# Kernel tuning notes

Measured on AMD Instinct MI355X. Metric: run time of the kernel, lower is better.

## Reference

```python
import jax, jax.numpy as jnp
import numpy as np

V = 100000
NNZ = 1600000
B = 4
C_IN = 64
C_HID = 128
C_OUT = 64
K = 4
BN_EPS = 1e-5


def cheb_conv(x, rows, cols, vals, W, b):
    # x: (B, Cin, V); W: (K, Cin, Cout); b: (Cout,)
    Bn, Cin, Vn = x.shape
    Kn = W.shape[0]

    def spmm(y):  # y: (V, F) -> L @ y via edge-list scatter-add
        return jax.ops.segment_sum(vals[:, None] * y[cols], rows, num_segments=Vn)

    x0 = jnp.transpose(x, (2, 0, 1)).reshape(Vn, Bn * Cin)  # (V, B*Cin)
    xs = [x0]
    if Kn > 1:
        x1 = spmm(x0)
        xs.append(x1)
        for _ in range(2, Kn):
            x2 = 2.0 * spmm(x1) - x0  # Chebyshev recurrence
            xs.append(x2)
            x0, x1 = x1, x2
    Xk = jnp.stack(xs, 0).reshape(Kn, Vn, Bn, Cin)  # (K, V, B, Cin)
    out = jnp.einsum('kvbi,kio->bov', Xk, W)  # (B, Cout, V)
    return out + b[None, :, None]


def batch_norm(x, gamma, beta):
    # BatchNorm1d on (B, C, V): stats over (B, V), biased variance (training mode)
    mean = jnp.mean(x, axis=(0, 2), keepdims=True)
    var = jnp.mean(jnp.square(x - mean), axis=(0, 2), keepdims=True)
    xn = (x - mean) * jax.lax.rsqrt(var + BN_EPS)
    return xn * gamma[None, :, None] + beta[None, :, None]


def setup_inputs() -> dict:
    key = jax.random.key(0)
    ks = jax.random.split(key, 8)
    x = jax.random.normal(ks[0], (B, C_IN, V), dtype=jnp.float32)
    lap_rows = jax.random.randint(ks[1], (NNZ,), 0, V, dtype=jnp.int32)
    lap_cols = jax.random.randint(ks[2], (NNZ,), 0, V, dtype=jnp.int32)
    # scale so the effective Laplacian spectral norm is ~O(1) (Chebyshev assumes rescaled L)
    lap_vals = jax.random.normal(ks[3], (NNZ,), dtype=jnp.float32) * 0.01
    w1 = jax.random.normal(ks[4], (K, C_IN, C_HID), dtype=jnp.float32) * (1.0 / np.sqrt(K * C_IN))
    b1 = jnp.zeros((C_HID,), dtype=jnp.float32)
    bn_gamma = jnp.ones((C_HID,), dtype=jnp.float32)
    bn_beta = jnp.zeros((C_HID,), dtype=jnp.float32)
    w2 = jax.random.normal(ks[5], (K, C_HID, C_OUT), dtype=jnp.float32) * (1.0 / np.sqrt(K * C_HID))
    b2 = jnp.zeros((C_OUT,), dtype=jnp.float32)
    return {"x": x, "lap_rows": lap_rows, "lap_cols": lap_cols, "lap_vals": lap_vals,
            "w1": w1, "b1": b1, "bn_gamma": bn_gamma, "bn_beta": bn_beta,
            "w2": w2, "b2": b2}


def reference(x, lap_rows, lap_cols, lap_vals, w1, b1, bn_gamma, bn_beta, w2, b2):
    out = cheb_conv(x, lap_rows, lap_cols, lap_vals, w1, b1)
    out = jax.nn.relu(out)
    out = batch_norm(out, bn_gamma, bn_beta)
    out = cheb_conv(out, lap_rows, lap_cols, lap_vals, w2, b2)
    # in_channels == out_channels -> resizer is Identity
    return jax.nn.relu(out + x)
```

## Files before the change

### kernel.cpp

```cpp
#include <hip/hip_runtime.h>

#define V 100000
#define NNZ 1600000

typedef unsigned short ushort_t;
typedef unsigned int uint_t;
typedef __attribute__((ext_vector_type(4))) float f32x4;
typedef __attribute__((ext_vector_type(8))) short bf16x8;

__device__ __forceinline__ float bf2f(ushort_t u) {
    union { uint_t i; float f; } x; x.i = ((uint_t)u) << 16; return x.f;
}
__device__ __forceinline__ ushort_t f2bf(float f) {
    union { float f; uint_t i; } x; x.f = f;
    uint_t u = x.i;
    return (ushort_t)((u + 0x7fffu + ((u >> 16) & 1u)) >> 16);
}
__device__ __forceinline__ float blo(uint_t u) {
    union { uint_t i; float f; } x; x.i = u << 16; return x.f;
}
__device__ __forceinline__ float bhi(uint_t u) {
    union { uint_t i; float f; } x; x.i = u & 0xffff0000u; return x.f;
}
__device__ __forceinline__ uint_t pk(float a, float b) {
    return (uint_t)f2bf(a) | ((uint_t)f2bf(b) << 16);
}
__device__ __forceinline__ void unpack8(uint4 u, float* f) {
    f[0] = blo(u.x); f[1] = bhi(u.x); f[2] = blo(u.y); f[3] = bhi(u.y);
    f[4] = blo(u.z); f[5] = bhi(u.z); f[6] = blo(u.w); f[7] = bhi(u.w);
}
__device__ __forceinline__ uint4 pack8(const float* f) {
    uint4 u;
    u.x = pk(f[0], f[1]); u.y = pk(f[2], f[3]);
    u.z = pk(f[4], f[5]); u.w = pk(f[6], f[7]);
    return u;
}

__global__ void diag_k(float* __restrict__ out, float code) {
    if (threadIdx.x == 0 && blockIdx.x == 0) out[0] = code;
}

__global__ __launch_bounds__(256) void pack_x0_k(const float* __restrict__ x,
                                                 ushort_t* __restrict__ x0) {
    __shared__ float tile[32][33];
    int v0 = blockIdx.x * 32, j0 = blockIdx.y * 32;
    int tx = threadIdx.x & 31, ty = threadIdx.x >> 5;
    for (int jj = ty; jj < 32; jj += 8)
        tile[jj][tx] = x[(size_t)(j0 + jj) * V + v0 + tx];
    __syncthreads();
    for (int vv = ty; vv < 32; vv += 8)
        x0[(size_t)(v0 + vv) * 256 + j0 + tx] = f2bf(tile[tx][vv]);
}

__global__ __launch_bounds__(256) void prep_w_k(const float* __restrict__ w1,
                                                const float* __restrict__ w2,
                                                ushort_t* __restrict__ wp1,
                                                ushort_t* __restrict__ wp2) {
    int idx = blockIdx.x * 256 + threadIdx.x;
    if (idx < 32768) {
        int f = idx;
        int j = f & 7, ch = (f >> 3) & 127, q = (f >> 10) & 3, kb = (f >> 12) & 3, L = (f >> 14) & 1;
        int k = kb * 32 + q * 8 + j;
        int t = L * 2 + (k >> 6), i = k & 63;
        wp1[idx] = f2bf(w1[((size_t)t * 64 + i) * 128 + ch]);
    } else {
        int f = idx - 32768;
        int j = f & 7, o = (f >> 3) & 63, q = (f >> 9) & 3, kb = (f >> 11) & 3, t = (f >> 13) & 3;
        int k = kb * 32 + q * 8 + j;
        wp2[f] = f2bf(w2[((size_t)t * 128 + k) * 64 + o]);
    }
}

__global__ __launch_bounds__(256) void hist_k(const int* __restrict__ rows,
                                              int* __restrict__ counts) {
    int e = blockIdx.x * 256 + threadIdx.x;
    atomicAdd(&counts[rows[e]], 1);
}

__global__ __launch_bounds__(256) void scan1_k(const int* __restrict__ counts,
                                               int* __restrict__ bsums) {
    __shared__ int sd[256];
    int t = threadIdx.x;
    int v = blockIdx.x * 256 + t;
    sd[t] = (v < V) ? counts[v] : 0;
    __syncthreads();
    for (int s = 128; s > 0; s >>= 1) {
        if (t < s) sd[t] += sd[t + s];
        __syncthreads();
    }
    if (t == 0) bsums[blockIdx.x] = sd[0];
}

__global__ __launch_bounds__(512) void scan2_k(int* __restrict__ bsums, int nb) {
    __shared__ int sd[512];
    int t = threadIdx.x;
    int v = (t < nb) ? bsums[t] : 0;
    sd[t] = v;
    __syncthreads();
    for (int off = 1; off < 512; off <<= 1) {
        int a = (t >= off) ? sd[t - off] : 0;
        __syncthreads();
        sd[t] += a;
        __syncthreads();
    }
    if (t < nb) bsums[t] = sd[t] - v;
}

__global__ __launch_bounds__(256) void scan3_k(const int* __restrict__ counts,
                                               const int* __restrict__ bsums,
                                               int* __restrict__ rowptr,
                                               int* __restrict__ cursor) {
    __shared__ int sd[256];
    int t = threadIdx.x;
    int v = blockIdx.x * 256 + t;
    int c = (v < V) ? counts[v] : 0;
    sd[t] = c;
    __syncthreads();
    for (int off = 1; off < 256; off <<= 1) {
        int a = (t >= off) ? sd[t - off] : 0;
        __syncthreads();
        sd[t] += a;
        __syncthreads();
    }
    if (v < V) {
        int start = bsums[blockIdx.x] + sd[t] - c;
        rowptr[v] = start;
        cursor[v] = start;
    }
    if (v == 0) rowptr[V] = NNZ;
}

__global__ __launch_bounds__(256) void scatter_k(const int* __restrict__ rows,
                                                 const int* __restrict__ cols,
                                                 const float* __restrict__ vals,
                                                 int* __restrict__ cursor,
                                                 int2* __restrict__ edges) {
    int e = blockIdx.x * 256 + threadIdx.x;
    int r = rows[e];
    int pos = atomicAdd(&cursor[r], 1);
    edges[pos] = make_int2(cols[e], __float_as_int(vals[e]));
}

__global__ __launch_bounds__(256) void spmm_wave(const int* __restrict__ rowptr,
                                                 const int2* __restrict__ edges,
                                                 const ushort_t* __restrict__ y,
                                                 const ushort_t* __restrict__ z,
                                                 float alpha, float beta,
                                                 ushort_t* __restrict__ out) {
    int v = (blockIdx.x * 256 + threadIdx.x) >> 6;
    if (v >= V) return;
    int l = threadIdx.x & 63;
    const ushort_t* yl = y + l * 4;

    float a0 = 0.f, a1 = 0.f, a2 = 0.f, a3 = 0.f;
    int e0 = rowptr[v], e1 = rowptr[v + 1];
    int e = e0;
    for (; e + 8 <= e1; e += 8) {
        int2 ed[8];
#pragma unroll
        for (int i = 0; i < 8; ++i) ed[i] = edges[e + i];
        uint2 u[8];
#pragma unroll
        for (int i = 0; i < 8; ++i) u[i] = *(const uint2*)(yl + (size_t)ed[i].x * 256);
#pragma unroll
        for (int i = 0; i < 8; ++i) {
            float wv = __int_as_float(ed[i].y);
            a0 += wv * blo(u[i].x);
            a1 += wv * bhi(u[i].x);
            a2 += wv * blo(u[i].y);
            a3 += wv * bhi(u[i].y);
        }
    }
    auto masked4 = [&](int base, int cnt) {
        int2 ed[4];
#pragma unroll
        for (int i = 0; i < 4; ++i) ed[i] = edges[i < cnt ? base + i : e0];
        uint2 u[4];
#pragma unroll
        for (int i = 0; i < 4; ++i) u[i] = *(const uint2*)(yl + (size_t)ed[i].x * 256);
#pragma unroll
        for (int i = 0; i < 4; ++i) {
            float wv = (i < cnt) ? __int_as_float(ed[i].y) : 0.f;
            a0 += wv * blo(u[i].x);
            a1 += wv * bhi(u[i].x);
            a2 += wv * blo(u[i].y);
            a3 += wv * bhi(u[i].y);
        }
    };
    int rem = e1 - e;
    if (rem > 0) masked4(e, rem > 4 ? 4 : rem);
    if (rem > 4) masked4(e + 4, rem - 4);

    float r0 = alpha * a0, r1 = alpha * a1, r2 = alpha * a2, r3 = alpha * a3;
    if (z) {
        uint2 t = *(const uint2*)(z + (size_t)v * 256 + l * 4);
        r0 += beta * blo(t.x);
        r1 += beta * bhi(t.x);
        r2 += beta * blo(t.y);
        r3 += beta * bhi(t.y);
    }
    uint2 st;
    st.x = (uint_t)f2bf(r0) | ((uint_t)f2bf(r1) << 16);
    st.y = (uint_t)f2bf(r2) | ((uint_t)f2bf(r3) << 16);
    *(uint2*)(out + (size_t)v * 256 + l * 4) = st;
}

__global__ __launch_bounds__(256) void gemm1_mfma(const ushort_t* __restrict__ t0,
                                                  const ushort_t* __restrict__ t1,
                                                  const ushort_t* __restrict__ wp,
                                                  const float* __restrict__ b1,
                                                  ushort_t* __restrict__ rb,
                                                  float* __restrict__ stats,
                                                  int first, int last) {
    __shared__ float smem[64 * 130];
    __shared__ float s_sum[128];
    __shared__ float s_sq[128];
    int tid = threadIdx.x;
    int l = tid & 63, w = tid >> 6;
    int q = l >> 4, n16 = l & 15;
    int b = blockIdx.y;
    int v0 = blockIdx.x * 64;
    if (last && tid < 128) { s_sum[tid] = 0.f; s_sq[tid] = 0.f; }
    int vrow = v0 + w * 16 + n16;
    int vc = vrow < V ? vrow : V - 1;

    f32x4 acc[8];
#pragma unroll
    for (int ct = 0; ct < 8; ++ct) acc[ct] = (f32x4){0.f, 0.f, 0.f, 0.f};

#pragma unroll
    for (int kb = 0; kb < 4; ++kb) {
        const ushort_t* tab = (kb < 2) ? t0 : t1;
        bf16x8 a = *(const bf16x8*)(tab + (size_t)vc * 256 + b * 64 + (kb & 1) * 32 + q * 8);
#pragma unroll
        for (int ct = 0; ct < 8; ++ct) {
            bf16x8 bf = *(const bf16x8*)(wp + (size_t)(((kb * 4 + q) * 128) + ct * 16 + n16) * 8);
            acc[ct] = __builtin_amdgcn_mfma_f32_16x16x32_bf16(a, bf, acc[ct], 0, 0, 0);
        }
    }

#pragma unroll
    for (int ct = 0; ct < 8; ++ct)
#pragma unroll
        for (int r = 0; r < 4; ++r)
            smem[(w * 16 + q * 4 + r) * 130 + ct * 16 + n16] = acc[ct][r];
    __syncthreads();

    int chunk = tid & 15;
    int rbase = tid >> 4;
    int ch0 = chunk * 8;
    float bc[8];
    if (last) {
#pragma unroll
        for (int j = 0; j < 8; ++j) bc[j] = b1[ch0 + j];
    }
    float csum[8], csq[8];
#pragma unroll
    for (int j = 0; j < 8; ++j) { csum[j] = 0.f; csq[j] = 0.f; }
#pragma unroll
    for (int k = 0; k < 4; ++k) {
        int row = rbase + k * 16;
        int v = v0 + row;
        bool valid = v < V;
        float vals[8];
#pragma unroll
        for (int j = 0; j < 8; ++j) vals[j] = smem[row * 130 + ch0 + j];
        ushort_t* p = rb + (size_t)(valid ? v : 0) * 512 + b * 128 + ch0;
        if (!first && valid) {
            uint4 old = *(const uint4*)p;
            float of[8];
            unpack8(old, of);
#pragma unroll
            for (int j = 0; j < 8; ++j) vals[j] += of[j];
        }
        if (last) {
#pragma unroll
            for (int j = 0; j < 8; ++j) vals[j] = fmaxf(vals[j] + bc[j], 0.f);
            if (valid) {
#pragma unroll
                for (int j = 0; j < 8; ++j) {
                    csum[j] += vals[j];
                    csq[j] += vals[j] * vals[j];
                }
            }
        }
        if (valid) *(uint4*)p = pack8(vals);
    }

    if (last) {
#pragma unroll
        for (int j = 0; j < 8; ++j) {
            csum[j] += __shfl_xor(csum[j], 16);
            csum[j] += __shfl_xor(csum[j], 32);
            csq[j] += __shfl_xor(csq[j], 16);
            csq[j] += __shfl_xor(csq[j], 32);
        }
        if (l < 16) {
#pragma unroll
            for (int j = 0; j < 8; ++j) {
                atomicAdd(&s_sum[ch0 + j], csum[j]);
                atomicAdd(&s_sq[ch0 + j], csq[j]);
            }
        }
        __syncthreads();
        if (tid < 128) {
            atomicAdd(&stats[tid], s_sum[tid]);
            atomicAdd(&stats[128 + tid], s_sq[tid]);
        }
    }
}

__global__ void finalize_k(const float* __restrict__ stats,
                           const float* __restrict__ gamma,
                           const float* __restrict__ beta,
                           float* __restrict__ ss) {
    int c = threadIdx.x;
    float n = (float)(4 * V);
    float mean = stats[c] / n;
    float var = stats[128 + c] / n - mean * mean;
    float inv = rsqrtf(var + 1e-5f);
    float sc = gamma[c] * inv;
    ss[c] = sc;
    ss[128 + c] = beta[c] - mean * sc;
}

__global__ __launch_bounds__(256) void gemmC_mfma(const ushort_t* __restrict__ rb,
                                                  const ushort_t* __restrict__ wp,
                                                  const ushort_t* __restrict__ S,
                                                  const float* __restrict__ ss,
                                                  ushort_t* __restrict__ P) {
    __shared__ float s_ss[256];
    __shared__ float smem[64 * 66];
    int tid = threadIdx.x;
    s_ss[tid] = ss[tid];
    __syncthreads();
    int l = tid & 63, w = tid >> 6;
    int q = l >> 4, n16 = l & 15;
    int b = blockIdx.y;
    int v0 = blockIdx.x * 64;
    int vrow = v0 + w * 16 + n16;
    int vc = vrow < V ? vrow : V - 1;

    f32x4 acc[4];
#pragma unroll
    for (int ct = 0; ct < 4; ++ct) acc[ct] = (f32x4){0.f, 0.f, 0.f, 0.f};

#pragma unroll
    for (int kb = 0; kb < 4; ++kb) {
        int chl = kb * 32 + q * 8;
        bf16x8 a = *(const bf16x8*)(rb + (size_t)vc * 512 + b * 128 + chl);
#pragma unroll
        for (int j = 0; j < 8; ++j) {
            float f = bf2f((ushort_t)a[j]) * s_ss[chl + j] + s_ss[128 + chl + j];
            a[j] = (short)f2bf(f);
        }
#pragma unroll
        for (int ct = 0; ct < 4; ++ct) {
            bf16x8 bf = *(const bf16x8*)(wp + (size_t)(((kb * 4 + q) * 64) + ct * 16 + n16) * 8);
            acc[ct] = __builtin_amdgcn_mfma_f32_16x16x32_bf16(a, bf, acc[ct], 0, 0, 0);
        }
    }

#pragma unroll
    for (int ct = 0; ct < 4; ++ct)
#pragma unroll
        for (int r = 0; r < 4; ++r)
            smem[(w * 16 + q * 4 + r) * 66 + ct * 16 + n16] = acc[ct][r];
    __syncthreads();

#pragma unroll
    for (int k = 0; k < 2; ++k) {
        int seg = tid + k * 256;
        int row = seg >> 3;
        int o0 = (seg & 7) * 8;
        int v = v0 + row;
        if (v >= V) continue;
        float vals[8];
#pragma unroll
        for (int j = 0; j < 8; ++j) vals[j] = smem[row * 66 + o0 + j];
        size_t idx = (size_t)v * 256 + b * 64 + o0;
        if (S) {
            uint4 sv = *(const uint4*)(S + idx);
            float sf[8];
            unpack8(sv, sf);
#pragma unroll
            for (int j = 0; j < 8; ++j) vals[j] += sf[j];
        }
        *(uint4*)(P + idx) = pack8(vals);
    }
}

__global__ __launch_bounds__(256) void gemm2_final(const ushort_t* __restrict__ rb,
                                                   const ushort_t* __restrict__ wp,
                                                   const ushort_t* __restrict__ Tb,
                                                   const float* __restrict__ b2,
                                                   const float* __restrict__ xres,
                                                   const float* __restrict__ ss,
                                                   float* __restrict__ out) {
    __shared__ float s_ss[256];
    __shared__ float smem[128 * 65];
    int tid = threadIdx.x;
    s_ss[tid] = ss[tid];
    int l = tid & 63, w = tid >> 6;
    int q = l >> 4, n16 = l & 15;
    int b = blockIdx.y;
    int v0 = blockIdx.x * 128;

#pragma unroll
    for (int k = 0; k < 4; ++k) {
        int seg = tid + k * 256;
        int row = seg >> 3;
        int o0 = (seg & 7) * 8;
        float tv[8];
        if (v0 + row < V) {
            uint4 t = *(const uint4*)(Tb + (size_t)(v0 + row) * 256 + b * 64 + o0);
            unpack8(t, tv);
        } else {
#pragma unroll
            for (int j = 0; j < 8; ++j) tv[j] = 0.f;
        }
#pragma unroll
        for (int j = 0; j < 8; ++j) smem[row * 65 + o0 + j] = tv[j];
    }
    __syncthreads();

    f32x4 acc[4][2];
#pragma unroll
    for (int rt = 0; rt < 4; ++rt)
#pragma unroll
        for (int c = 0; c < 2; ++c) acc[rt][c] = (f32x4){0.f, 0.f, 0.f, 0.f};

    int vcol[2];
#pragma unroll
    for (int c = 0; c < 2; ++c) {
        int v = v0 + (w * 2 + c) * 16 + n16;
        vcol[c] = v < V ? v : V - 1;
    }

#pragma unroll
    for (int kb = 0; kb < 4; ++kb) {
        int chl = kb * 32 + q * 8;
        bf16x8 bfr[2];
#pragma unroll
        for (int c = 0; c < 2; ++c) {
            bf16x8 t = *(const bf16x8*)(rb + (size_t)vcol[c] * 512 + b * 128 + chl);
#pragma unroll
            for (int j = 0; j < 8; ++j) {
                float f = bf2f((ushort_t)t[j]) * s_ss[chl + j] + s_ss[128 + chl + j];
                t[j] = (short)f2bf(f);
            }
            bfr[c] = t;
        }
#pragma unroll
        for (int rt = 0; rt < 4; ++rt) {
            bf16x8 af = *(const bf16x8*)(wp + (size_t)(((kb * 4 + q) * 64) + rt * 16 + n16) * 8);
#pragma unroll
            for (int c = 0; c < 2; ++c)
                acc[rt][c] = __builtin_amdgcn_mfma_f32_16x16x32_bf16(af, bfr[c], acc[rt][c], 0, 0, 0);
        }
    }

#pragma unroll
    for (int rt = 0; rt < 4; ++rt)
#pragma unroll
        for (int c = 0; c < 2; ++c) {
            int vl = (w * 2 + c) * 16 + n16;
#pragma unroll
            for (int r = 0; r < 4; ++r)
                acc[rt][c][r] += smem[vl * 65 + rt * 16 + q * 4 + r];
        }
    __syncthreads();

#pragma unroll
    for (int rt = 0; rt < 4; ++rt)
#pragma unroll
        for (int c = 0; c < 2; ++c) {
            int vl = (w * 2 + c) * 16 + n16;
#pragma unroll
            for (int r = 0; r < 4; ++r)
                smem[(rt * 16 + q * 4 + r) * 130 + vl] = acc[rt][c][r];
        }
    __syncthreads();

    int o = tid >> 2, m = tid & 3;
    float bias = b2[o];
    const float* xr = xres + (size_t)(b * 64 + o) * V + v0;
    float* op = out + (size_t)(b * 64 + o) * V + v0;
#pragma unroll
    for (int j = 0; j < 8; ++j) {
        int voff = m * 4 + j * 16;
        if (v0 + voff < V) {
            f32x4 xv = *(const f32x4*)(xr + voff);
            f32x4 res;
#pragma unroll
            for (int i = 0; i < 4; ++i)
                res[i] = fmaxf(smem[o * 130 + voff + i] + bias + xv[i], 0.f);
            *(f32x4*)(op + voff) = res;
        }
    }
}

extern "C" void kernel_launch(void* const* d_in, const int* in_sizes, int n_in,
                              void* d_out, int out_size, void* d_ws, size_t ws_size,
                              hipStream_t stream) {
    const float* x = (const float*)d_in[0];
    const int* lap_rows = (const int*)d_in[1];
    const int* lap_cols = (const int*)d_in[2];
    const float* lap_vals = (const float*)d_in[3];
    const float* w1 = (const float*)d_in[4];
    const float* b1 = (const float*)d_in[5];
    const float* bn_gamma = (const float*)d_in[6];
    const float* bn_beta = (const float*)d_in[7];
    const float* w2 = (const float*)d_in[8];
    const float* b2 = (const float*)d_in[9];
    float* out = (float*)d_out;

    char* ws = (char*)d_ws;
    size_t off = 0;
    auto alloc = [&](size_t bytes) {
        size_t r = off;
        off = (off + bytes + 255) & ~(size_t)255;
        return r;
    };
    size_t reg1_off = alloc((size_t)V * 512 * 2);
    size_t rb_off   = alloc((size_t)V * 512 * 2);
    size_t sc_off   = alloc((size_t)V * 256 * 2);
    size_t rp_off   = alloc((size_t)(V + 1) * 4);
    size_t cur_off  = alloc((size_t)V * 4);
    size_t ed_off   = alloc((size_t)NNZ * 8);
    size_t st_off   = alloc(256 * 4);
    size_t ss_off   = alloc(256 * 4);
    size_t bs_off   = alloc(512 * 4);
    size_t wp1_off  = alloc(32768 * 2);
    size_t wp2_off  = alloc(32768 * 2);

    if (ws_size < off) {
        diag_k<<<1, 64, 0, stream>>>(out, 1000.f + (float)(ws_size >> 20));
        return;
    }

    ushort_t* slotA = (ushort_t*)(ws + reg1_off);
    ushort_t* slotB = slotA + (size_t)V * 256;
    ushort_t* slotC = (ushort_t*)(ws + sc_off);
    ushort_t* rb = (ushort_t*)(ws + rb_off);
    int* rowptr = (int*)(ws + rp_off);
    int* cursor = (int*)(ws + cur_off);
    int2* edges = (int2*)(ws + ed_off);
    float* stats = (float*)(ws + st_off);
    float* ss = (float*)(ws + ss_off);
    int* bsums = (int*)(ws + bs_off);
    ushort_t* wp1 = (ushort_t*)(ws + wp1_off);
    ushort_t* wp2 = (ushort_t*)(ws + wp2_off);

    const int NB = (V + 255) / 256;
    const int SG = (V + 3) / 4;
    const ushort_t* nullu = (const ushort_t*)nullptr;

    hipMemsetAsync(cursor, 0, (size_t)V * 4, stream);
    hipMemsetAsync(stats, 0, 256 * 4, stream);

    pack_x0_k<<<dim3(V / 32, 8), 256, 0, stream>>>(x, slotA);
    prep_w_k<<<256, 256, 0, stream>>>(w1, w2, wp1, wp2);
    hist_k<<<NNZ / 256, 256, 0, stream>>>(lap_rows, cursor);
    scan1_k<<<NB, 256, 0, stream>>>(cursor, bsums);
    scan2_k<<<1, 512, 0, stream>>>(bsums, NB);
    scan3_k<<<NB, 256, 0, stream>>>(cursor, bsums, rowptr, cursor);
    scatter_k<<<NNZ / 256, 256, 0, stream>>>(lap_rows, lap_cols, lap_vals, cursor, edges);

    dim3 g1((V + 63) / 64, 4);
    dim3 g2((V + 127) / 128, 4);

    spmm_wave<<<SG, 256, 0, stream>>>(rowptr, edges, slotA, nullu, 1.f, 0.f, slotB);
    gemm1_mfma<<<g1, 256, 0, stream>>>(slotA, slotB, wp1, b1, rb, stats, 1, 0);
    spmm_wave<<<SG, 256, 0, stream>>>(rowptr, edges, slotB, slotA, 2.f, -1.f, slotA);
    spmm_wave<<<SG, 256, 0, stream>>>(rowptr, edges, slotA, slotB, 2.f, -1.f, slotB);
    gemm1_mfma<<<g1, 256, 0, stream>>>(slotA, slotB, wp1 + 16384, b1, rb, stats, 0, 1);

    finalize_k<<<1, 128, 0, stream>>>(stats, bn_gamma, bn_beta, ss);

    gemmC_mfma<<<g1, 256, 0, stream>>>(rb, wp2 + 3 * 8192, nullu, ss, slotA);
    spmm_wave<<<SG, 256, 0, stream>>>(rowptr, edges, slotA, nullu, 2.f, 0.f, slotB);
    gemmC_mfma<<<g1, 256, 0, stream>>>(rb, wp2 + 2 * 8192, slotB, ss, slotC);
    spmm_wave<<<SG, 256, 0, stream>>>(rowptr, edges, slotC, slotA, 2.f, -1.f, slotA);
    gemmC_mfma<<<g1, 256, 0, stream>>>(rb, wp2 + 1 * 8192, slotA, ss, slotB);
    spmm_wave<<<SG, 256, 0, stream>>>(rowptr, edges, slotB, slotC, 1.f, -1.f, slotC);
    gemm2_final<<<g2, 256, 0, stream>>>(rb, wp2, slotC, b2, x, ss, out);
}
```

Before: 1.505 ms.

## Shrink LDS in gemm kernels, split BN stats into separate pass, scalarize spmm row bounds

The spmm row index and edge bounds become wave-uniform via readfirstlane, so they can live in scalar registers. gemm1 now stages its output through LDS in two halves with a smaller buffer, and the BatchNorm statistics move out of it into a new stats_k kernel that rereads rb. gemm2_final drops its transpose-through-LDS epilogue and writes the residual output straight from MFMA accumulators, with bf16 T staged as packed words. The smaller LDS footprint is meant to raise occupancy, at the cost of an extra full pass over rb and less-coalesced output stores.

```diff
diff --git a/kernel.cpp b/kernel.cpp
--- a/kernel.cpp
+++ b/kernel.cpp
@@ -147,13 +147,14 @@
                                                  const ushort_t* __restrict__ z,
                                                  float alpha, float beta,
                                                  ushort_t* __restrict__ out) {
-    int v = (blockIdx.x * 256 + threadIdx.x) >> 6;
+    int v = __builtin_amdgcn_readfirstlane((blockIdx.x * 256 + threadIdx.x) >> 6);
     if (v >= V) return;
     int l = threadIdx.x & 63;
     const ushort_t* yl = y + l * 4;
 
     float a0 = 0.f, a1 = 0.f, a2 = 0.f, a3 = 0.f;
-    int e0 = rowptr[v], e1 = rowptr[v + 1];
+    int e0 = __builtin_amdgcn_readfirstlane(rowptr[v]);
+    int e1 = __builtin_amdgcn_readfirstlane(rowptr[v + 1]);
     int e = e0;
     for (; e + 8 <= e1; e += 8) {
         int2 ed[8];
@@ -210,17 +211,13 @@
                                                   const ushort_t* __restrict__ wp,
                                                   const float* __restrict__ b1,
                                                   ushort_t* __restrict__ rb,
-                                                  float* __restrict__ stats,
                                                   int first, int last) {
-    __shared__ float smem[64 * 130];
-    __shared__ float s_sum[128];
-    __shared__ float s_sq[128];
+    __shared__ float smem[64 * 66];
     int tid = threadIdx.x;
     int l = tid & 63, w = tid >> 6;
     int q = l >> 4, n16 = l & 15;
     int b = blockIdx.y;
     int v0 = blockIdx.x * 64;
-    if (last && tid < 128) { s_sum[tid] = 0.f; s_sq[tid] = 0.f; }
     int vrow = v0 + w * 16 + n16;
     int vc = vrow < V ? vrow : V - 1;
 
@@ -239,74 +236,83 @@
         }
     }
 
-#pragma unroll
-    for (int ct = 0; ct < 8; ++ct)
-#pragma unroll
-        for (int r = 0; r < 4; ++r)
-            smem[(w * 16 + q * 4 + r) * 130 + ct * 16 + n16] = acc[ct][r];
-    __syncthreads();
-
-    int chunk = tid & 15;
-    int rbase = tid >> 4;
-    int ch0 = chunk * 8;
-    float bc[8];
-    if (last) {
-#pragma unroll
-        for (int j = 0; j < 8; ++j) bc[j] = b1[ch0 + j];
-    }
-    float csum[8], csq[8];
-#pragma unroll
-    for (int j = 0; j < 8; ++j) { csum[j] = 0.f; csq[j] = 0.f; }
-#pragma unroll
-    for (int k = 0; k < 4; ++k) {
-        int row = rbase + k * 16;
-        int v = v0 + row;
-        bool valid = v < V;
-        float vals[8];
-#pragma unroll
-        for (int j = 0; j < 8; ++j) vals[j] = smem[row * 130 + ch0 + j];
-        ushort_t* p = rb + (size_t)(valid ? v : 0) * 512 + b * 128 + ch0;
-        if (!first && valid) {
-            uint4 old = *(const uint4*)p;
-            float of[8];
-            unpack8(old, of);
-#pragma unroll
-            for (int j = 0; j < 8; ++j) vals[j] += of[j];
-        }
+    int row_d = tid >> 3;
+    int c8 = tid & 7;
+#pragma unroll
+    for (int h = 0; h < 2; ++h) {
+        if (h) __syncthreads();
+#pragma unroll
+        for (int ct = 0; ct < 4; ++ct)
+#pragma unroll
+            for (int r = 0; r < 4; ++r)
+                smem[(w * 16 + q * 4 + r) * 66 + ct * 16 + n16] = acc[h * 4 + ct][r];
+        __syncthreads();
+
+        int ch0 = h * 64 + c8 * 8;
+        float bc[8];
         if (last) {
 #pragma unroll
-            for (int j = 0; j < 8; ++j) vals[j] = fmaxf(vals[j] + bc[j], 0.f);
-            if (valid) {
-#pragma unroll
-                for (int j = 0; j < 8; ++j) {
-                    csum[j] += vals[j];
-                    csq[j] += vals[j] * vals[j];
-                }
+            for (int j = 0; j < 8; ++j) bc[j] = b1[ch0 + j];
+        }
+#pragma unroll
+        for (int k = 0; k < 2; ++k) {
+            int row = row_d + k * 32;
+            int v = v0 + row;
+            bool valid = v < V;
+            float vals[8];
+#pragma unroll
+            for (int j = 0; j < 8; ++j) vals[j] = smem[row * 66 + c8 * 8 + j];
+            ushort_t* p = rb + (size_t)(valid ? v : 0) * 512 + b * 128 + ch0;
+            if (!first && valid) {
+                uint4 old = *(const uint4*)p;
+                float of[8];
+                unpack8(old, of);
+#pragma unroll
+                for (int j = 0; j < 8; ++j) vals[j] += of[j];
             }
-        }
-        if (valid) *(uint4*)p = pack8(vals);
-    }
-
-    if (last) {
+            if (last) {
+#pragma unroll
+                for (int j = 0; j < 8; ++j) vals[j] = fmaxf(vals[j] + bc[j], 0.f);
+            }
+            if (valid) *(uint4*)p = pack8(vals);
+        }
+    }
+}
+
+__global__ __launch_bounds__(256) void stats_k(const ushort_t* __restrict__ rb,
+                                               float* __restrict__ stats) {
+    __shared__ float s_sum[128], s_sq[128];
+    int tid = threadIdx.x;
+    if (tid < 128) { s_sum[tid] = 0.f; s_sq[tid] = 0.f; }
+    __syncthreads();
+    int g = tid & 15, t16 = tid >> 4;
+    float cs[8], cq[8];
+#pragma unroll
+    for (int j = 0; j < 8; ++j) { cs[j] = 0.f; cq[j] = 0.f; }
+    for (int idx = blockIdx.x * 16 + t16; idx < V * 4; idx += 256 * 16) {
+        int v = idx >> 2, bb = idx & 3;
+        uint4 u = *(const uint4*)(rb + (size_t)v * 512 + bb * 128 + g * 8);
+        float f[8];
+        unpack8(u, f);
+#pragma unroll
+        for (int j = 0; j < 8; ++j) { cs[j] += f[j]; cq[j] += f[j] * f[j]; }
+    }
+#pragma unroll
+    for (int j = 0; j < 8; ++j) {
+        cs[j] += __shfl_xor(cs[j], 16); cs[j] += __shfl_xor(cs[j], 32);
+        cq[j] += __shfl_xor(cq[j], 16); cq[j] += __shfl_xor(cq[j], 32);
+    }
+    if ((tid & 63) < 16) {
 #pragma unroll
         for (int j = 0; j < 8; ++j) {
-            csum[j] += __shfl_xor(csum[j], 16);
-            csum[j] += __shfl_xor(csum[j], 32);
-            csq[j] += __shfl_xor(csq[j], 16);
-            csq[j] += __shfl_xor(csq[j], 32);
-        }
-        if (l < 16) {
-#pragma unroll
-            for (int j = 0; j < 8; ++j) {
-                atomicAdd(&s_sum[ch0 + j], csum[j]);
-                atomicAdd(&s_sq[ch0 + j], csq[j]);
-            }
-        }
-        __syncthreads();
-        if (tid < 128) {
-            atomicAdd(&stats[tid], s_sum[tid]);
-            atomicAdd(&stats[128 + tid], s_sq[tid]);
-        }
+            atomicAdd(&s_sum[g * 8 + j], cs[j]);
+            atomicAdd(&s_sq[g * 8 + j], cq[j]);
+        }
+    }
+    __syncthreads();
+    if (tid < 128) {
+        atomicAdd(&stats[tid], s_sum[tid]);
+        atomicAdd(&stats[128 + tid], s_sq[tid]);
     }
 }
 
@@ -398,9 +404,11 @@
                                                    const float* __restrict__ ss,
                                                    float* __restrict__ out) {
     __shared__ float s_ss[256];
-    __shared__ float smem[128 * 65];
+    __shared__ float s_b2[64];
+    __shared__ uint_t s_tb[128 * 36];
     int tid = threadIdx.x;
     s_ss[tid] = ss[tid];
+    if (tid < 64) s_b2[tid] = b2[tid];
     int l = tid & 63, w = tid >> 6;
     int q = l >> 4, n16 = l & 15;
     int b = blockIdx.y;
@@ -409,18 +417,10 @@
 #pragma unroll
     for (int k = 0; k < 4; ++k) {
         int seg = tid + k * 256;
-        int row = seg >> 3;
-        int o0 = (seg & 7) * 8;
-        float tv[8];
-        if (v0 + row < V) {
-            uint4 t = *(const uint4*)(Tb + (size_t)(v0 + row) * 256 + b * 64 + o0);
-            unpack8(t, tv);
-        } else {
-#pragma unroll
-            for (int j = 0; j < 8; ++j) tv[j] = 0.f;
-        }
-#pragma unroll
-        for (int j = 0; j < 8; ++j) smem[row * 65 + o0 + j] = tv[j];
+        int row = seg >> 3, c = seg & 7;
+        uint4 t = make_uint4(0u, 0u, 0u, 0u);
+        if (v0 + row < V) t = *(const uint4*)(Tb + (size_t)(v0 + row) * 256 + b * 64 + c * 8);
+        *(uint4*)&s_tb[row * 36 + c * 4] = t;
     }
     __syncthreads();
 
@@ -465,39 +465,19 @@
 #pragma unroll
         for (int c = 0; c < 2; ++c) {
             int vl = (w * 2 + c) * 16 + n16;
-#pragma unroll
-            for (int r = 0; r < 4; ++r)
-                acc[rt][c][r] += smem[vl * 65 + rt * 16 + q * 4 + r];
-        }
-    __syncthreads();
-
-#pragma unroll
-    for (int rt = 0; rt < 4; ++rt)
-#pragma unroll
-        for (int c = 0; c < 2; ++c) {
-            int vl = (w * 2 + c) * 16 + n16;
-#pragma unroll
-            for (int r = 0; r < 4; ++r)
-                smem[(rt * 16 + q * 4 + r) * 130 + vl] = acc[rt][c][r];
-        }
-    __syncthreads();
-
-    int o = tid >> 2, m = tid & 3;
-    float bias = b2[o];
-    const float* xr = xres + (size_t)(b * 64 + o) * V + v0;
-    float* op = out + (size_t)(b * 64 + o) * V + v0;
-#pragma unroll
-    for (int j = 0; j < 8; ++j) {
-        int voff = m * 4 + j * 16;
-        if (v0 + voff < V) {
-            f32x4 xv = *(const f32x4*)(xr + voff);
-            f32x4 res;
-#pragma unroll
-            for (int i = 0; i < 4; ++i)
-                res[i] = fmaxf(smem[o * 130 + voff + i] + bias + xv[i], 0.f);
-            *(f32x4*)(op + voff) = res;
-        }
-    }
+            int v = v0 + vl;
+            bool valid = v < V;
+            int vv = valid ? v : 0;
+#pragma unroll
+            for (int r = 0; r < 4; ++r) {
+                int o = rt * 16 + q * 4 + r;
+                uint_t pr = s_tb[vl * 36 + rt * 8 + q * 2 + (r >> 1)];
+                float tb = (r & 1) ? bhi(pr) : blo(pr);
+                size_t idx = (size_t)(b * 64 + o) * V + vv;
+                float val = acc[rt][c][r] + tb + s_b2[o] + xres[idx];
+                if (valid) out[idx] = fmaxf(val, 0.f);
+            }
+        }
 }
 
 extern "C" void kernel_launch(void* const* d_in, const int* in_sizes, int n_in,
@@ -571,11 +551,12 @@
     dim3 g2((V + 127) / 128, 4);
 
     spmm_wave<<<SG, 256, 0, stream>>>(rowptr, edges, slotA, nullu, 1.f, 0.f, slotB);
-    gemm1_mfma<<<g1, 256, 0, stream>>>(slotA, slotB, wp1, b1, rb, stats, 1, 0);
+    gemm1_mfma<<<g1, 256, 0, stream>>>(slotA, slotB, wp1, b1, rb, 1, 0);
     spmm_wave<<<SG, 256, 0, stream>>>(rowptr, edges, slotB, slotA, 2.f, -1.f, slotA);
     spmm_wave<<<SG, 256, 0, stream>>>(rowptr, edges, slotA, slotB, 2.f, -1.f, slotB);
-    gemm1_mfma<<<g1, 256, 0, stream>>>(slotA, slotB, wp1 + 16384, b1, rb, stats, 0, 1);
-
+    gemm1_mfma<<<g1, 256, 0, stream>>>(slotA, slotB, wp1 + 16384, b1, rb, 0, 1);
+
+    stats_k<<<256, 256, 0, stream>>>(rb, stats);
     finalize_k<<<1, 128, 0, stream>>>(stats, bn_gamma, bn_beta, ss);
 
     gemmC_mfma<<<g1, 256, 0, stream>>>(rb, wp2 + 3 * 8192, nullu, ss, slotA);
```

New measurement: 1.430 ms. -5.0%, faster.
